# Kernel optimization log

Measured on AMD Instinct MI355X. Metric: run time of the kernel, lower is better.

The kernel has to match this reference:

```python
import jax, jax.numpy as jnp
import numpy as np

R = 2
K = 2 * R + 1  # kernel size 5


def _patches(x, axis):
    """Zero-padded sliding-window patches along `axis` for a [B,H,W,1] tensor.
    Mimics tf.image.extract_patches with SAME padding (zeros). Returns [B,H,W,K]."""
    pad = [(0, 0)] * 4
    pad[axis] = (R, R)
    xp = jnp.pad(x, pad)
    n = x.shape[axis]
    slices = [jax.lax.slice_in_dim(xp, i, i + n, axis=axis) for i in range(K)]
    return jnp.concatenate(slices, axis=-1)  # channel dim is 1 -> stacks taps


def _do_blur(bright_p, dark_p, depths_p, depths, spatial_dist, depth_var, spatial_var):
    # depth-guided weight, per tap
    rel = jnp.minimum(jnp.abs(depths_p / depths - 1.0), 1.0)
    w = jnp.exp(-jnp.square(rel) / (2.0 * depth_var)) * \
        jnp.exp(-jnp.square(spatial_dist) / (2.0 * spatial_var))
    w = w / jnp.sum(w, axis=-1, keepdims=True)
    b = jnp.sum(bright_p * w, axis=-1, keepdims=True)
    d = jnp.sum(dark_p * w, axis=-1, keepdims=True)
    return b, d


def _custom_pow(a, b):
    return jnp.exp(b * jnp.log(jnp.maximum(a, 1e-8)))


def setup_inputs() -> dict:
    key = jax.random.key(0)
    k1, k2, k3 = jax.random.split(key, 3)
    B, H, W = 8, 1024, 1024
    bright = jax.random.uniform(k1, (B, H, W, 1), dtype=jnp.float32)
    dark = jax.random.uniform(k2, (B, H, W, 1), dtype=jnp.float32)
    # depths are divided by; keep strictly positive
    depths = 0.1 + 0.9 * jax.random.uniform(k3, (B, H, W, 1), dtype=jnp.float32)
    return {
        "bright": bright,
        "dark": dark,
        "depths": depths,
        "depth_variance": jnp.float32(0.0004),
        "spatial_variance": jnp.float32(13.16),
        "dev_exponent": jnp.float32(0.3),
        "dark_epsilon": jnp.float32(0.375),
        "contrast_enhance": jnp.float32(0.95),
    }


def reference(bright, dark, depths, depth_variance, spatial_variance,
              dev_exponent, dark_epsilon, contrast_enhance):
    spatial_dist = jnp.arange(-R, R + 1, dtype=jnp.float32).reshape(1, 1, 1, K)
    # horizontal pass (along W = axis 2)
    bx, dx, zx = _patches(bright, 2), _patches(dark, 2), _patches(depths, 2)
    bright_x, dark_x = _do_blur(bx, dx, zx, depths, spatial_dist,
                                depth_variance, spatial_variance)
    # vertical pass (along H = axis 1) on horizontally-blurred values
    by, dy, zy = _patches(bright_x, 1), _patches(dark_x, 1), _patches(depths, 1)
    bright_mean, dark_mean = _do_blur(by, dy, zy, depths, spatial_dist,
                                      depth_variance, spatial_variance)
    # contrast-aware blend of bright/dark channels
    dev_bright = _custom_pow(jnp.abs(bright - bright_mean), dev_exponent)
    dev_dark = _custom_pow(jnp.abs(dark - dark_mean), dev_exponent)
    dev_dark = jnp.maximum(dev_dark, dark_epsilon)
    dev_bright = dev_bright * contrast_enhance
    wsum = dev_bright + dev_dark
    dev_bright = dev_bright / wsum
    dev_dark = dev_dark / wsum
    return dev_dark * bright + dev_bright * dark
```

## Files before the change

kernel.cpp:

```cpp
#include <hip/hip_runtime.h>

#define TH 4
#define W_ 1024
#define H_ 1024

__device__ __forceinline__ float wexp1(float zp, float iz, float kd, float kspat) {
    const float u = fmaf(zp, iz, -1.0f);
    return __builtin_amdgcn_exp2f(fmaf(u * kd, u, kspat));
}

__device__ __forceinline__ void blur5(
    float zm2, float zm1, float zc, float zp1, float zp2,
    float bm2, float bm1, float bc, float bp1, float bp2,
    float dm2, float dm1, float dc, float dp1, float dp2,
    float kd, float ks1, float ks4,
    float& ob, float& od)
{
    const float iz = __builtin_amdgcn_rcpf(zc);
    const float w0 = wexp1(zm2, iz, kd, ks4);
    const float w1 = wexp1(zm1, iz, kd, ks1);
    const float w3 = wexp1(zp1, iz, kd, ks1);
    const float w4 = wexp1(zp2, iz, kd, ks4);
    const float wr = __builtin_amdgcn_rcpf(1.0f + w0 + w1 + w3 + w4);
    ob = fmaf(w0, bm2, fmaf(w1, bm1, fmaf(w3, bp1, fmaf(w4, bp2, bc)))) * wr;
    od = fmaf(w0, dm2, fmaf(w1, dm1, fmaf(w3, dp1, fmaf(w4, dp2, dc)))) * wr;
}

__device__ __forceinline__ float blend1(float bc, float dc, float bm, float dm,
                                        float de, float dke, float ce) {
    const float devb = __builtin_amdgcn_exp2f(
        de * __builtin_amdgcn_logf(fmaxf(fabsf(bc - bm), 1e-8f))) * ce;
    const float devd = fmaxf(__builtin_amdgcn_exp2f(
        de * __builtin_amdgcn_logf(fmaxf(fabsf(dc - dm), 1e-8f))), dke);
    const float wr = __builtin_amdgcn_rcpf(devb + devd);
    return fmaf(devd, bc, devb * dc) * wr;
}

__device__ __forceinline__ void stage_row(
    int gy, const float* __restrict__ bB, const float* __restrict__ dB,
    const float* __restrict__ zB,
    int c, int colL2, int colR2, bool eL, bool eR,
    float kd, float ks1, float ks4,
    float4& sb, float4& sd, float4& sz)
{
    if ((unsigned)gy < (unsigned)H_) {
        const size_t ro = (size_t)gy * W_;
        const float2 lb = *(const float2*)(bB + ro + colL2);
        const float4 cb = *(const float4*)(bB + ro + c);
        const float2 rb = *(const float2*)(bB + ro + colR2);
        const float2 ld = *(const float2*)(dB + ro + colL2);
        const float4 cd = *(const float4*)(dB + ro + c);
        const float2 rd = *(const float2*)(dB + ro + colR2);
        float2 lz = *(const float2*)(zB + ro + colL2);
        const float4 cz = *(const float4*)(zB + ro + c);
        float2 rz = *(const float2*)(zB + ro + colR2);
        if (eL) { lz.x = 1e18f; lz.y = 1e18f; }
        if (eR) { rz.x = 1e18f; rz.y = 1e18f; }
        blur5(lz.x, lz.y, cz.x, cz.y, cz.z,  lb.x, lb.y, cb.x, cb.y, cb.z,
              ld.x, ld.y, cd.x, cd.y, cd.z,  kd, ks1, ks4, sb.x, sd.x);
        blur5(lz.y, cz.x, cz.y, cz.z, cz.w,  lb.y, cb.x, cb.y, cb.z, cb.w,
              ld.y, cd.x, cd.y, cd.z, cd.w,  kd, ks1, ks4, sb.y, sd.y);
        blur5(cz.x, cz.y, cz.z, cz.w, rz.x,  cb.x, cb.y, cb.z, cb.w, rb.x,
              cd.x, cd.y, cd.z, cd.w, rd.x,  kd, ks1, ks4, sb.z, sd.z);
        blur5(cz.y, cz.z, cz.w, rz.x, rz.y,  cb.y, cb.z, cb.w, rb.x, rb.y,
              cd.y, cd.z, cd.w, rd.x, rd.y,  kd, ks1, ks4, sb.w, sd.w);
        sz = cz;
    } else {
        sb = make_float4(0.f, 0.f, 0.f, 0.f);
        sd = make_float4(0.f, 0.f, 0.f, 0.f);
        sz = make_float4(0.f, 0.f, 0.f, 0.f);
    }
}

#define STEP(S, S0, S1, S2, S3, S4, I)                                        \
  {                                                                           \
    stage_row(y0 + (I) - 2, bB, dB, zB, c, colL2, colR2, eL, eR,              \
              kd, ks1, ks4, pb[S], pd[S], pz[S]);                             \
    float4 bm, dm;                                                            \
    blur5(pz[S0].x, pz[S1].x, pz[S2].x, pz[S3].x, pz[S4].x,                   \
          pb[S0].x, pb[S1].x, pb[S2].x, pb[S3].x, pb[S4].x,                   \
          pd[S0].x, pd[S1].x, pd[S2].x, pd[S3].x, pd[S4].x,                   \
          kd, ks1, ks4, bm.x, dm.x);                                          \
    blur5(pz[S0].y, pz[S1].y, pz[S2].y, pz[S3].y, pz[S4].y,                   \
          pb[S0].y, pb[S1].y, pb[S2].y, pb[S3].y, pb[S4].y,                   \
          pd[S0].y, pd[S1].y, pd[S2].y, pd[S3].y, pd[S4].y,                   \
          kd, ks1, ks4, bm.y, dm.y);                                          \
    blur5(pz[S0].z, pz[S1].z, pz[S2].z, pz[S3].z, pz[S4].z,                   \
          pb[S0].z, pb[S1].z, pb[S2].z, pb[S3].z, pb[S4].z,                   \
          pd[S0].z, pd[S1].z, pd[S2].z, pd[S3].z, pd[S4].z,                   \
          kd, ks1, ks4, bm.z, dm.z);                                          \
    blur5(pz[S0].w, pz[S1].w, pz[S2].w, pz[S3].w, pz[S4].w,                   \
          pb[S0].w, pb[S1].w, pb[S2].w, pb[S3].w, pb[S4].w,                   \
          pd[S0].w, pd[S1].w, pd[S2].w, pd[S3].w, pd[S4].w,                   \
          kd, ks1, ks4, bm.w, dm.w);                                          \
    const size_t oo = (size_t)(y0 + (I) - 4) * W_ + c;                        \
    const float4 rb4 = *(const float4*)(bB + oo);                             \
    const float4 rd4 = *(const float4*)(dB + oo);                             \
    float4 res;                                                               \
    res.x = blend1(rb4.x, rd4.x, bm.x, dm.x, de, dke, ce);                    \
    res.y = blend1(rb4.y, rd4.y, bm.y, dm.y, de, dke, ce);                    \
    res.z = blend1(rb4.z, rd4.z, bm.z, dm.z, de, dke, ce);                    \
    res.w = blend1(rb4.w, rd4.w, bm.w, dm.w, de, dke, ce);                    \
    *(float4*)(outB + oo) = res;                                              \
  }

__global__ __launch_bounds__(256, 4)
void bilateral_fused(const float* __restrict__ bright,
                     const float* __restrict__ dark,
                     const float* __restrict__ depths,
                     const float* __restrict__ p_dv,
                     const float* __restrict__ p_sv,
                     const float* __restrict__ p_de,
                     const float* __restrict__ p_deps,
                     const float* __restrict__ p_ce,
                     float* __restrict__ out)
{
    const float LOG2E = 1.44269504088896340736f;
    const float kd  = -LOG2E / (2.0f * p_dv[0]);
    const float ks  = -LOG2E / (2.0f * p_sv[0]);
    const float de  = p_de[0];
    const float dke = p_deps[0];
    const float ce  = p_ce[0];
    const float ks1 = ks;
    const float ks4 = 4.0f * ks;

    const int t  = threadIdx.x;
    const int c  = 4 * t;
    const int y0 = blockIdx.y * TH;

    const size_t plane = (size_t)H_ * W_;
    const float* bB = bright + (size_t)blockIdx.z * plane;
    const float* dB = dark   + (size_t)blockIdx.z * plane;
    const float* zB = depths + (size_t)blockIdx.z * plane;
    float*     outB = out    + (size_t)blockIdx.z * plane;

    const int  colL2 = max(c - 2, 0);
    const int  colR2 = min(c + 4, W_ - 2);
    const bool eL = (c == 0);
    const bool eR = (c + 4 >= W_);

    float4 pb[5], pd[5], pz[5];

    stage_row(y0 - 2, bB, dB, zB, c, colL2, colR2, eL, eR, kd, ks1, ks4, pb[0], pd[0], pz[0]);
    stage_row(y0 - 1, bB, dB, zB, c, colL2, colR2, eL, eR, kd, ks1, ks4, pb[1], pd[1], pz[1]);
    stage_row(y0 + 0, bB, dB, zB, c, colL2, colR2, eL, eR, kd, ks1, ks4, pb[2], pd[2], pz[2]);
    stage_row(y0 + 1, bB, dB, zB, c, colL2, colR2, eL, eR, kd, ks1, ks4, pb[3], pd[3], pz[3]);

    STEP(4, 0, 1, 2, 3, 4,  4)
    STEP(0, 1, 2, 3, 4, 0,  5)
    STEP(1, 2, 3, 4, 0, 1,  6)
    STEP(2, 3, 4, 0, 1, 2,  7)
}

extern "C" void kernel_launch(void* const* d_in, const int* in_sizes, int n_in,
                              void* d_out, int out_size, void* d_ws, size_t ws_size,
                              hipStream_t stream)
{
    const float* bright = (const float*)d_in[0];
    const float* dark   = (const float*)d_in[1];
    const float* depths = (const float*)d_in[2];
    const float* p_dv   = (const float*)d_in[3];
    const float* p_sv   = (const float*)d_in[4];
    const float* p_de   = (const float*)d_in[5];
    const float* p_deps = (const float*)d_in[6];
    const float* p_ce   = (const float*)d_in[7];
    float* out = (float*)d_out;

    const int B = in_sizes[0] / (H_ * W_);

    dim3 grid(1, H_ / TH, B);
    dim3 block(256);
    bilateral_fused<<<grid, block, 0, stream>>>(bright, dark, depths,
                                                p_dv, p_sv, p_de, p_deps, p_ce,
                                                out);
}
```

Measured before the change: 162.5 us.

## Double rows per block and software-prefetch next row's raw data

Each block now handles 8 output rows instead of 4, which cuts the redundant 4-row halo recomputation of the horizontal blur. Row loads are split from the horizontal blur so the next row's global loads are issued before the current row's maths, and the output-row loads are hoisted ahead of the vertical blur. This aims to hide memory latency and reduce halo overhead. In exchange it raises register pressure and halves the number of blocks, which may lower occupancy or latency hiding.

```diff
diff --git a/kernel.cpp b/kernel.cpp
--- a/kernel.cpp
+++ b/kernel.cpp
@@ -1,6 +1,6 @@
 #include <hip/hip_runtime.h>
 
-#define TH 4
+#define TH 8
 #define W_ 1024
 #define H_ 1024
 
@@ -36,35 +36,55 @@
     return fmaf(devd, bc, devb * dc) * wr;
 }
 
-__device__ __forceinline__ void stage_row(
+struct Raw {
+    float2 lb, rb, ld, rd, lz, rz;
+    float4 cb, cd, cz;
+};
+
+__device__ __forceinline__ void load_raw(
     int gy, const float* __restrict__ bB, const float* __restrict__ dB,
-    const float* __restrict__ zB,
-    int c, int colL2, int colR2, bool eL, bool eR,
+    const float* __restrict__ zB, int c, int colL2, int colR2, Raw& r)
+{
+    if ((unsigned)gy < (unsigned)H_) {
+        const size_t ro = (size_t)gy * W_;
+        r.lz = *(const float2*)(zB + ro + colL2);
+        r.cz = *(const float4*)(zB + ro + c);
+        r.rz = *(const float2*)(zB + ro + colR2);
+        r.lb = *(const float2*)(bB + ro + colL2);
+        r.cb = *(const float4*)(bB + ro + c);
+        r.rb = *(const float2*)(bB + ro + colR2);
+        r.ld = *(const float2*)(dB + ro + colL2);
+        r.cd = *(const float4*)(dB + ro + c);
+        r.rd = *(const float2*)(dB + ro + colR2);
+    }
+}
+
+__device__ __forceinline__ void hblur_raw(
+    int gy, const Raw& r, bool eL, bool eR,
     float kd, float ks1, float ks4,
     float4& sb, float4& sd, float4& sz)
 {
     if ((unsigned)gy < (unsigned)H_) {
-        const size_t ro = (size_t)gy * W_;
-        const float2 lb = *(const float2*)(bB + ro + colL2);
-        const float4 cb = *(const float4*)(bB + ro + c);
-        const float2 rb = *(const float2*)(bB + ro + colR2);
-        const float2 ld = *(const float2*)(dB + ro + colL2);
-        const float4 cd = *(const float4*)(dB + ro + c);
-        const float2 rd = *(const float2*)(dB + ro + colR2);
-        float2 lz = *(const float2*)(zB + ro + colL2);
-        const float4 cz = *(const float4*)(zB + ro + c);
-        float2 rz = *(const float2*)(zB + ro + colR2);
+        float2 lz = r.lz, rz = r.rz;
         if (eL) { lz.x = 1e18f; lz.y = 1e18f; }
         if (eR) { rz.x = 1e18f; rz.y = 1e18f; }
-        blur5(lz.x, lz.y, cz.x, cz.y, cz.z,  lb.x, lb.y, cb.x, cb.y, cb.z,
-              ld.x, ld.y, cd.x, cd.y, cd.z,  kd, ks1, ks4, sb.x, sd.x);
-        blur5(lz.y, cz.x, cz.y, cz.z, cz.w,  lb.y, cb.x, cb.y, cb.z, cb.w,
-              ld.y, cd.x, cd.y, cd.z, cd.w,  kd, ks1, ks4, sb.y, sd.y);
-        blur5(cz.x, cz.y, cz.z, cz.w, rz.x,  cb.x, cb.y, cb.z, cb.w, rb.x,
-              cd.x, cd.y, cd.z, cd.w, rd.x,  kd, ks1, ks4, sb.z, sd.z);
-        blur5(cz.y, cz.z, cz.w, rz.x, rz.y,  cb.y, cb.z, cb.w, rb.x, rb.y,
-              cd.y, cd.z, cd.w, rd.x, rd.y,  kd, ks1, ks4, sb.w, sd.w);
-        sz = cz;
+        blur5(lz.x, lz.y, r.cz.x, r.cz.y, r.cz.z,
+              r.lb.x, r.lb.y, r.cb.x, r.cb.y, r.cb.z,
+              r.ld.x, r.ld.y, r.cd.x, r.cd.y, r.cd.z,
+              kd, ks1, ks4, sb.x, sd.x);
+        blur5(lz.y, r.cz.x, r.cz.y, r.cz.z, r.cz.w,
+              r.lb.y, r.cb.x, r.cb.y, r.cb.z, r.cb.w,
+              r.ld.y, r.cd.x, r.cd.y, r.cd.z, r.cd.w,
+              kd, ks1, ks4, sb.y, sd.y);
+        blur5(r.cz.x, r.cz.y, r.cz.z, r.cz.w, rz.x,
+              r.cb.x, r.cb.y, r.cb.z, r.cb.w, r.rb.x,
+              r.cd.x, r.cd.y, r.cd.z, r.cd.w, r.rd.x,
+              kd, ks1, ks4, sb.z, sd.z);
+        blur5(r.cz.y, r.cz.z, r.cz.w, rz.x, rz.y,
+              r.cb.y, r.cb.z, r.cb.w, r.rb.x, r.rb.y,
+              r.cd.y, r.cd.z, r.cd.w, r.rd.x, r.rd.y,
+              kd, ks1, ks4, sb.w, sd.w);
+        sz = r.cz;
     } else {
         sb = make_float4(0.f, 0.f, 0.f, 0.f);
         sd = make_float4(0.f, 0.f, 0.f, 0.f);
@@ -72,10 +92,19 @@
     }
 }
 
-#define STEP(S, S0, S1, S2, S3, S4, I)                                        \
+#define WSTEP(S, I)                                                           \
   {                                                                           \
-    stage_row(y0 + (I) - 2, bB, dB, zB, c, colL2, colR2, eL, eR,              \
-              kd, ks1, ks4, pb[S], pd[S], pz[S]);                             \
+    hblur_raw(y0 + (I) - 2, R, eL, eR, kd, ks1, ks4, pb[S], pd[S], pz[S]);    \
+    load_raw(y0 + (I) - 1, bB, dB, zB, c, colL2, colR2, R);                   \
+  }
+
+#define FSTEP(S, S0, S1, S2, S3, S4, I, PREF)                                 \
+  {                                                                           \
+    hblur_raw(y0 + (I) - 2, R, eL, eR, kd, ks1, ks4, pb[S], pd[S], pz[S]);    \
+    if (PREF) load_raw(y0 + (I) - 1, bB, dB, zB, c, colL2, colR2, R);         \
+    const size_t oo = (size_t)(y0 + (I) - 4) * W_ + c;                        \
+    const float4 rb4 = *(const float4*)(bB + oo);                             \
+    const float4 rd4 = *(const float4*)(dB + oo);                             \
     float4 bm, dm;                                                            \
     blur5(pz[S0].x, pz[S1].x, pz[S2].x, pz[S3].x, pz[S4].x,                   \
           pb[S0].x, pb[S1].x, pb[S2].x, pb[S3].x, pb[S4].x,                   \
@@ -93,9 +122,6 @@
           pb[S0].w, pb[S1].w, pb[S2].w, pb[S3].w, pb[S4].w,                   \
           pd[S0].w, pd[S1].w, pd[S2].w, pd[S3].w, pd[S4].w,                   \
           kd, ks1, ks4, bm.w, dm.w);                                          \
-    const size_t oo = (size_t)(y0 + (I) - 4) * W_ + c;                        \
-    const float4 rb4 = *(const float4*)(bB + oo);                             \
-    const float4 rd4 = *(const float4*)(dB + oo);                             \
     float4 res;                                                               \
     res.x = blend1(rb4.x, rd4.x, bm.x, dm.x, de, dke, ce);                    \
     res.y = blend1(rb4.y, rd4.y, bm.y, dm.y, de, dke, ce);                    \
@@ -140,16 +166,23 @@
     const bool eR = (c + 4 >= W_);
 
     float4 pb[5], pd[5], pz[5];
-
-    stage_row(y0 - 2, bB, dB, zB, c, colL2, colR2, eL, eR, kd, ks1, ks4, pb[0], pd[0], pz[0]);
-    stage_row(y0 - 1, bB, dB, zB, c, colL2, colR2, eL, eR, kd, ks1, ks4, pb[1], pd[1], pz[1]);
-    stage_row(y0 + 0, bB, dB, zB, c, colL2, colR2, eL, eR, kd, ks1, ks4, pb[2], pd[2], pz[2]);
-    stage_row(y0 + 1, bB, dB, zB, c, colL2, colR2, eL, eR, kd, ks1, ks4, pb[3], pd[3], pz[3]);
-
-    STEP(4, 0, 1, 2, 3, 4,  4)
-    STEP(0, 1, 2, 3, 4, 0,  5)
-    STEP(1, 2, 3, 4, 0, 1,  6)
-    STEP(2, 3, 4, 0, 1, 2,  7)
+    Raw R;
+
+    load_raw(y0 - 2, bB, dB, zB, c, colL2, colR2, R);
+
+    WSTEP(0, 0)
+    WSTEP(1, 1)
+    WSTEP(2, 2)
+    WSTEP(3, 3)
+
+    FSTEP(4, 0, 1, 2, 3, 4,  4, 1)
+    FSTEP(0, 1, 2, 3, 4, 0,  5, 1)
+    FSTEP(1, 2, 3, 4, 0, 1,  6, 1)
+    FSTEP(2, 3, 4, 0, 1, 2,  7, 1)
+    FSTEP(3, 4, 0, 1, 2, 3,  8, 1)
+    FSTEP(4, 0, 1, 2, 3, 4,  9, 1)
+    FSTEP(0, 1, 2, 3, 4, 0, 10, 1)
+    FSTEP(1, 2, 3, 4, 0, 1, 11, 0)
 }
 
 extern "C" void kernel_launch(void* const* d_in, const int* in_sizes, int n_in,
```

Measured after the change: 155.5 us. 1.04x faster.

## Stage halo rows through LDS with async global_load_lds and taller row tiles

Applied to the files above, without the earlier changes.

Replaces the per-thread overlapping float2/float4 global loads of each input row with asynchronous global-to-LDS DMA into a triple-buffered shared row ring. The horizontal blur then reads its neighbours from LDS, and vmcnt waits plus barriers pipeline the load of the next row behind the compute on the current one. Rows per block rise from 4 to 8, which cuts the redundant vertical halo reads from 4 of 8 rows to 4 of 12. The cost is a block barrier per row, 36 KB of LDS per block that may lower occupancy, and hand-counted vmcnt values that must stay matched to the issue order.

```diff
diff --git a/kernel.cpp b/kernel.cpp
--- a/kernel.cpp
+++ b/kernel.cpp
@@ -1,8 +1,17 @@
 #include <hip/hip_runtime.h>
-
-#define TH 4
+#include <stdint.h>
+
+#define TH 8
 #define W_ 1024
 #define H_ 1024
+
+typedef __attribute__((address_space(3))) uint32_t lds_u32;
+typedef __attribute__((address_space(1))) const uint32_t glb_u32;
+
+__device__ __forceinline__ void dma16(const float* g, float* l) {
+    __builtin_amdgcn_global_load_lds((glb_u32*)(uintptr_t)g,
+                                     (lds_u32*)(uintptr_t)l, 16, 0, 0);
+}
 
 __device__ __forceinline__ float wexp1(float zp, float iz, float kd, float kspat) {
     const float u = fmaf(zp, iz, -1.0f);
@@ -36,24 +45,34 @@
     return fmaf(devd, bc, devb * dc) * wr;
 }
 
-__device__ __forceinline__ void stage_row(
+__device__ __forceinline__ void dma_row(
     int gy, const float* __restrict__ bB, const float* __restrict__ dB,
     const float* __restrict__ zB,
+    float* sZs, float* sBs, float* sDs, int c, int wb)
+{
+    const int gyc = min(max(gy, 0), H_ - 1);
+    const size_t ro = (size_t)gyc * W_;
+    dma16(zB + ro + c, sZs + wb);
+    dma16(bB + ro + c, sBs + wb);
+    dma16(dB + ro + c, sDs + wb);
+}
+
+__device__ __forceinline__ void hblur_lds(
+    int gy, const float* sZs, const float* sBs, const float* sDs,
     int c, int colL2, int colR2, bool eL, bool eR,
     float kd, float ks1, float ks4,
     float4& sb, float4& sd, float4& sz)
 {
     if ((unsigned)gy < (unsigned)H_) {
-        const size_t ro = (size_t)gy * W_;
-        const float2 lb = *(const float2*)(bB + ro + colL2);
-        const float4 cb = *(const float4*)(bB + ro + c);
-        const float2 rb = *(const float2*)(bB + ro + colR2);
-        const float2 ld = *(const float2*)(dB + ro + colL2);
-        const float4 cd = *(const float4*)(dB + ro + c);
-        const float2 rd = *(const float2*)(dB + ro + colR2);
-        float2 lz = *(const float2*)(zB + ro + colL2);
-        const float4 cz = *(const float4*)(zB + ro + c);
-        float2 rz = *(const float2*)(zB + ro + colR2);
+        float2 lz = *(const float2*)(sZs + colL2);
+        const float4 cz = *(const float4*)(sZs + c);
+        float2 rz = *(const float2*)(sZs + colR2);
+        const float2 lb = *(const float2*)(sBs + colL2);
+        const float4 cb = *(const float4*)(sBs + c);
+        const float2 rb = *(const float2*)(sBs + colR2);
+        const float2 ld = *(const float2*)(sDs + colL2);
+        const float4 cd = *(const float4*)(sDs + c);
+        const float2 rd = *(const float2*)(sDs + colR2);
         if (eL) { lz.x = 1e18f; lz.y = 1e18f; }
         if (eR) { rz.x = 1e18f; rz.y = 1e18f; }
         blur5(lz.x, lz.y, cz.x, cz.y, cz.z,  lb.x, lb.y, cb.x, cb.y, cb.z,
@@ -72,9 +91,28 @@
     }
 }
 
-#define STEP(S, S0, S1, S2, S3, S4, I)                                        \
+#define PHASE(N)                                                              \
+    asm volatile("s_waitcnt vmcnt(" #N ")" ::: "memory");                     \
+    __builtin_amdgcn_s_barrier();                                             \
+    asm volatile("" ::: "memory");
+
+#define WSTEP(S, CS, DS, K, N)                                                \
   {                                                                           \
-    stage_row(y0 + (I) - 2, bB, dB, zB, c, colL2, colR2, eL, eR,              \
+    dma_row(y0 + (K) - 1, bB, dB, zB, sZ[DS], sB[DS], sD[DS], c, wb);         \
+    PHASE(N)                                                                  \
+    hblur_lds(y0 + (K) - 2, sZ[CS], sB[CS], sD[CS], c, colL2, colR2, eL, eR,  \
+              kd, ks1, ks4, pb[S], pd[S], pz[S]);                             \
+  }
+
+#define FSTEP(S, S0, S1, S2, S3, S4, CS, DS, K, N, DODMA)                     \
+  {                                                                           \
+    const size_t oo = (size_t)(y0 + (K) - 4) * W_ + c;                        \
+    const float4 rb4 = *(const float4*)(bB + oo);                             \
+    const float4 rd4 = *(const float4*)(dB + oo);                             \
+    asm volatile("" ::: "memory");  \
+    if (DODMA) dma_row(y0 + (K) - 1, bB, dB, zB, sZ[DS], sB[DS], sD[DS], c, wb); \
+    PHASE(N)                                                                  \
+    hblur_lds(y0 + (K) - 2, sZ[CS], sB[CS], sD[CS], c, colL2, colR2, eL, eR,  \
               kd, ks1, ks4, pb[S], pd[S], pz[S]);                             \
     float4 bm, dm;                                                            \
     blur5(pz[S0].x, pz[S1].x, pz[S2].x, pz[S3].x, pz[S4].x,                   \
@@ -93,9 +131,6 @@
           pb[S0].w, pb[S1].w, pb[S2].w, pb[S3].w, pb[S4].w,                   \
           pd[S0].w, pd[S1].w, pd[S2].w, pd[S3].w, pd[S4].w,                   \
           kd, ks1, ks4, bm.w, dm.w);                                          \
-    const size_t oo = (size_t)(y0 + (I) - 4) * W_ + c;                        \
-    const float4 rb4 = *(const float4*)(bB + oo);                             \
-    const float4 rd4 = *(const float4*)(dB + oo);                             \
     float4 res;                                                               \
     res.x = blend1(rb4.x, rd4.x, bm.x, dm.x, de, dke, ce);                    \
     res.y = blend1(rb4.y, rd4.y, bm.y, dm.y, de, dke, ce);                    \
@@ -115,6 +150,10 @@
                      const float* __restrict__ p_ce,
                      float* __restrict__ out)
 {
+    __shared__ __attribute__((aligned(16))) float sZ[3][W_];
+    __shared__ __attribute__((aligned(16))) float sB[3][W_];
+    __shared__ __attribute__((aligned(16))) float sD[3][W_];
+
     const float LOG2E = 1.44269504088896340736f;
     const float kd  = -LOG2E / (2.0f * p_dv[0]);
     const float ks  = -LOG2E / (2.0f * p_sv[0]);
@@ -126,6 +165,7 @@
 
     const int t  = threadIdx.x;
     const int c  = 4 * t;
+    const int wb = (t >> 6) << 8;
     const int y0 = blockIdx.y * TH;
 
     const size_t plane = (size_t)H_ * W_;
@@ -141,15 +181,21 @@
 
     float4 pb[5], pd[5], pz[5];
 
-    stage_row(y0 - 2, bB, dB, zB, c, colL2, colR2, eL, eR, kd, ks1, ks4, pb[0], pd[0], pz[0]);
-    stage_row(y0 - 1, bB, dB, zB, c, colL2, colR2, eL, eR, kd, ks1, ks4, pb[1], pd[1], pz[1]);
-    stage_row(y0 + 0, bB, dB, zB, c, colL2, colR2, eL, eR, kd, ks1, ks4, pb[2], pd[2], pz[2]);
-    stage_row(y0 + 1, bB, dB, zB, c, colL2, colR2, eL, eR, kd, ks1, ks4, pb[3], pd[3], pz[3]);
-
-    STEP(4, 0, 1, 2, 3, 4,  4)
-    STEP(0, 1, 2, 3, 4, 0,  5)
-    STEP(1, 2, 3, 4, 0, 1,  6)
-    STEP(2, 3, 4, 0, 1, 2,  7)
+    dma_row(y0 - 2, bB, dB, zB, sZ[0], sB[0], sD[0], c, wb);
+
+    WSTEP(0, 0, 1, 0, 3)
+    WSTEP(1, 1, 2, 1, 3)
+    WSTEP(2, 2, 0, 2, 3)
+    WSTEP(3, 0, 1, 3, 3)
+
+    FSTEP(4, 0, 1, 2, 3, 4,  1, 2,  4, 5, 1)
+    FSTEP(0, 1, 2, 3, 4, 0,  2, 0,  5, 6, 1)
+    FSTEP(1, 2, 3, 4, 0, 1,  0, 1,  6, 6, 1)
+    FSTEP(2, 3, 4, 0, 1, 2,  1, 2,  7, 6, 1)
+    FSTEP(3, 4, 0, 1, 2, 3,  2, 0,  8, 6, 1)
+    FSTEP(4, 0, 1, 2, 3, 4,  0, 1,  9, 6, 1)
+    FSTEP(0, 1, 2, 3, 4, 0,  1, 2, 10, 6, 1)
+    FSTEP(1, 2, 3, 4, 0, 1,  2, 0, 11, 3, 0)
 }
 
 extern "C" void kernel_launch(void* const* d_in, const int* in_sizes, int n_in,
```

Result: no change. 161.2 us (-0.8%).
